# Optimization experiments

Measured on AMD Instinct MI355X. Metric: run time of the kernel, lower is better.

Reference implementation:

```python
import jax, jax.numpy as jnp
import numpy as np

N_EXPERTS = 8
TOPK = 2


def setup_inputs() -> dict:
    key = jax.random.key(0)
    k1, k2, k3, k4 = jax.random.split(key, 4)
    B, T, D, H, E = 2, 2048, 1024, 4096, N_EXPERTS
    s = 1.0 / np.sqrt(D)
    return {
        "x": jax.random.normal(k1, (B, T, D), dtype=jnp.float32),
        "W_gate": jax.random.normal(k2, (E, D), dtype=jnp.float32) * s,
        "W_fc": jax.random.normal(k3, (E, H, D), dtype=jnp.float32) * s,
        "W_proj": jax.random.normal(k4, (E, D, H), dtype=jnp.float32) * (1.0 / np.sqrt(H)),
    }


def reference(x, W_gate, W_fc, W_proj):
    B, T, D = x.shape
    E = W_gate.shape[0]
    N = B * T
    xf = x.reshape(N, D)

    # gating
    gate_logits = xf @ W_gate.T                       # [N, E]
    gate_probs = jax.nn.softmax(gate_logits, axis=-1)
    rw, eidx = jax.lax.top_k(gate_probs, TOPK)        # [N, K]
    rw = rw / jnp.sum(rw, axis=-1, keepdims=True)

    # exact dispatch: out[n] = sum_k rw[n,k] * MLP_{eidx[n,k]}(x[n])
    # loop over the small fixed expert count; each expert processes all tokens,
    # masked-combined by its per-token routing weight (same math as index_add dispatch).
    out = jnp.zeros_like(xf)
    for e in range(E):
        we = jnp.sum(jnp.where(eidx == e, rw, 0.0), axis=-1)     # [N]
        h = jnp.square(jax.nn.relu(xf @ W_fc[e].T))              # relu(x)^2, [N, H]
        out = out + (h @ W_proj[e].T) * we[:, None]

    # load-balance loss
    ones = jnp.ones((N * TOPK,), dtype=gate_probs.dtype)
    counts = jax.ops.segment_sum(ones, eidx.reshape(-1), num_segments=E)
    expert_freq = counts / N
    balance_loss = jnp.sum(gate_probs.mean(axis=0) * jax.lax.stop_gradient(expert_freq)) * E

    return out.reshape(B, T, D), balance_loss
```

## Files before the change

### kernel.cpp

```cpp
#include <hip/hip_runtime.h>
#include <hip/hip_bf16.h>
#include <math.h>

#define N_TOK 4096
#define D_DIM 1024
#define H_DIM 4096
#define E_NUM 8
#define NSLOT (N_TOK * 2)

typedef short bf16x8 __attribute__((ext_vector_type(8)));
typedef float f32x4 __attribute__((ext_vector_type(4)));


__device__ __forceinline__ unsigned short f2bf(float f) {
  unsigned int u = __float_as_uint(f);
  u += 0x7FFFu + ((u >> 16) & 1u);
  return (unsigned short)(u >> 16);
}

__device__ __forceinline__ void gld_lds16(const void* g, void* l) {
  __builtin_amdgcn_global_load_lds(
      (__attribute__((address_space(1))) void*)(g),
      (__attribute__((address_space(3))) void*)(l), 16, 0, 0);
}


__global__ void zero_init(float* __restrict__ p, int n4, int* __restrict__ ctrl) {
  int i = blockIdx.x * blockDim.x + threadIdx.x;
  if (i < n4) ((float4*)p)[i] = make_float4(0.f, 0.f, 0.f, 0.f);
  if (blockIdx.x == 0 && threadIdx.x < 64) ctrl[threadIdx.x] = 0;
}

__global__ void cvt_weights(const float* __restrict__ wfc, const float* __restrict__ wproj,
                            unsigned short* __restrict__ wfcb, unsigned short* __restrict__ wpjb) {
  const int L = 8388608;
  const int stride = gridDim.x * blockDim.x;
  for (int i = blockIdx.x * blockDim.x + threadIdx.x; i < 2 * L; i += stride) {
    const bool first = (i < L);
    const int j = first ? i : i - L;
    float4 v = first ? ((const float4*)wfc)[j] : ((const float4*)wproj)[j];
    ushort4 o;
    o.x = f2bf(v.x); o.y = f2bf(v.y); o.z = f2bf(v.z); o.w = f2bf(v.w);
    if (first) ((ushort4*)wfcb)[j] = o; else ((ushort4*)wpjb)[j] = o;
  }
}


__global__ void gating_kernel(const float* __restrict__ x,
                              const float* __restrict__ wg,
                              float* __restrict__ probs,
                              int* __restrict__ eidx,
                              float* __restrict__ rw,
                              unsigned short* __restrict__ xb) {
  __shared__ float4 wg_lds[2048];
  const int t = threadIdx.x;
  const int lane = t & 63;
  const int wave = t >> 6;

#pragma unroll
  for (int j = 0; j < 8; ++j)
    wg_lds[t + 256 * j] = ((const float4*)wg)[t + 256 * j];
  __syncthreads();

#pragma unroll
  for (int j = 0; j < 4; ++j) {
    const int n = blockIdx.x * 16 + wave * 4 + j;
    const float4* xr = (const float4*)(x + (size_t)n * D_DIM);
    ushort4* xw = (ushort4*)(xb + (size_t)n * D_DIM);

    float acc[E_NUM];
#pragma unroll
    for (int e = 0; e < E_NUM; ++e) acc[e] = 0.f;

#pragma unroll
    for (int i = 0; i < 4; ++i) {
      float4 xv = xr[lane + 64 * i];
      ushort4 xo;
      xo.x = f2bf(xv.x); xo.y = f2bf(xv.y); xo.z = f2bf(xv.z); xo.w = f2bf(xv.w);
      xw[lane + 64 * i] = xo;
#pragma unroll
      for (int e = 0; e < E_NUM; ++e) {
        float4 wv = wg_lds[e * 256 + lane + 64 * i];
        acc[e] += xv.x * wv.x + xv.y * wv.y + xv.z * wv.z + xv.w * wv.w;
      }
    }
#pragma unroll
    for (int m = 1; m < 64; m <<= 1) {
#pragma unroll
      for (int e = 0; e < E_NUM; ++e) acc[e] += __shfl_xor(acc[e], m, 64);
    }

    float mx = acc[0];
#pragma unroll
    for (int e = 1; e < E_NUM; ++e) mx = fmaxf(mx, acc[e]);
    float p[E_NUM], s = 0.f;
#pragma unroll
    for (int e = 0; e < E_NUM; ++e) { p[e] = __expf(acc[e] - mx); s += p[e]; }
    float inv = 1.f / s;

    if (lane < E_NUM) probs[(size_t)n * E_NUM + lane] = p[lane] * inv;

    if (lane == 0) {
      int i1 = 0;
#pragma unroll
      for (int e = 1; e < E_NUM; ++e) if (p[e] > p[i1]) i1 = e;
      int i2 = (i1 == 0) ? 1 : 0;
#pragma unroll
      for (int e = 0; e < E_NUM; ++e)
        if (e != i1 && p[e] > p[i2]) i2 = e;
      float p1 = p[i1], p2 = p[i2];
      float wsum = 1.f / (p1 + p2);
      eidx[n] = i1 | (i2 << 8);
      rw[2 * n] = p1 * wsum;
      rw[2 * n + 1] = p2 * wsum;
    }
  }
}

__global__ void reduce_route(const float* __restrict__ probs,
                             const int* __restrict__ eidx,
                             int* __restrict__ counts,
                             int* __restrict__ offsets,
                             float* __restrict__ loss) {
  const int t = threadIdx.x;
  float4 part = make_float4(0.f, 0.f, 0.f, 0.f);
  for (int j = 0; j < 32; ++j) {
    float4 v = ((const float4*)probs)[t + 256 * j];
    part.x += v.x; part.y += v.y; part.z += v.z; part.w += v.w;
  }
  int cnt[E_NUM];
#pragma unroll
  for (int e = 0; e < E_NUM; ++e) cnt[e] = 0;
  for (int j = 0; j < 16; ++j) {
    int pk = eidx[t + 256 * j];
    int e1 = pk & 255, e2 = pk >> 8;
#pragma unroll
    for (int e = 0; e < E_NUM; ++e) cnt[e] += (e1 == e) + (e2 == e);
  }

  __shared__ float redf[256 * E_NUM];
  __shared__ int redi[256 * E_NUM];
  const int eb = (t & 1) * 4;
#pragma unroll
  for (int e = 0; e < E_NUM; ++e) { redf[t * E_NUM + e] = 0.f; redi[t * E_NUM + e] = cnt[e]; }
  redf[t * E_NUM + eb + 0] = part.x;
  redf[t * E_NUM + eb + 1] = part.y;
  redf[t * E_NUM + eb + 2] = part.z;
  redf[t * E_NUM + eb + 3] = part.w;
  __syncthreads();
  for (int s = 128; s > 0; s >>= 1) {
    if (t < s) {
#pragma unroll
      for (int e = 0; e < E_NUM; ++e) {
        redf[t * E_NUM + e] += redf[(t + s) * E_NUM + e];
        redi[t * E_NUM + e] += redi[(t + s) * E_NUM + e];
      }
    }
    __syncthreads();
  }
  if (t == 0) {
    int o = 0;
    float L = 0.f;
    for (int e = 0; e < E_NUM; ++e) {
      int c = redi[e];
      counts[e] = c;
      offsets[e] = o;
      o += c;
      L += redf[e] * (float)c;
    }
    loss[0] = L * (float)E_NUM / ((float)N_TOK * (float)N_TOK);
  }
}

__global__ void scatter_kernel(const int* __restrict__ eidx, const float* __restrict__ rw,
                               const int* __restrict__ offsets, int* __restrict__ cursor,
                               int* __restrict__ tok_id, float* __restrict__ tok_w) {
  __shared__ int lcnt[E_NUM];
  __shared__ int lbase[E_NUM];
  const int t = threadIdx.x;
  const int n = blockIdx.x * 256 + t;
  if (t < E_NUM) lcnt[t] = 0;
  __syncthreads();
  int pk = eidx[n];
  int e1 = pk & 255, e2 = pk >> 8;
  int p1 = atomicAdd(&lcnt[e1], 1);
  int p2 = atomicAdd(&lcnt[e2], 1);
  __syncthreads();
  if (t < E_NUM) lbase[t] = atomicAdd(&cursor[t], lcnt[t]);
  __syncthreads();
  int d1 = offsets[e1] + lbase[e1] + p1;
  tok_id[d1] = n; tok_w[d1] = rw[2 * n];
  int d2 = offsets[e2] + lbase[e2] + p2;
  tok_id[d2] = n; tok_w[d2] = rw[2 * n + 1];
}


__launch_bounds__(256, 2)
__global__ void gemm_fc(const unsigned short* __restrict__ xb,
                        const unsigned short* __restrict__ wfc,
                        const int* __restrict__ tok_id,
                        const int* __restrict__ counts,
                        const int* __restrict__ offsets,
                        unsigned short* __restrict__ hbuf) {
  const int e = blockIdx.z;
  const int cnt = counts[e];
  const int mtile = blockIdx.y;
  if (mtile * 128 >= cnt) return;
  const int ntile = blockIdx.x;
  const int off = offsets[e];

  __shared__ __align__(16) unsigned short As[128 * 64];
  __shared__ __align__(16) unsigned short Bs[128 * 64];

  const int t = threadIdx.x;
  const int lane = t & 63;
  const int wave = t >> 6;
  const int wm = (wave >> 1) * 64;
  const int wn = (wave & 1) * 64;
  const int srow = t >> 3;
  const int seg = (t & 7) ^ (srow & 7);

  const unsigned short* aptr[4];
  const unsigned short* bptr[4];
#pragma unroll
  for (int p = 0; p < 4; ++p) {
    int r = mtile * 128 + p * 32 + srow;
    r = (r < cnt) ? r : (cnt - 1);
    int tok = tok_id[off + r];
    aptr[p] = xb + (size_t)tok * D_DIM + seg * 8;
    int br = ntile * 128 + p * 32 + srow;
    bptr[p] = wfc + ((size_t)e * H_DIM + br) * D_DIM + seg * 8;
  }

  f32x4 acc[4][4];
#pragma unroll
  for (int i = 0; i < 4; ++i)
#pragma unroll
    for (int j = 0; j < 4; ++j) acc[i][j] = (f32x4){0.f, 0.f, 0.f, 0.f};

  const int frow_a = wm + (lane & 15);
  const int frow_b = wn + (lane & 15);
  const int q = lane >> 4;
  const int csw = lane & 7;

  for (int k0 = 0; k0 < D_DIM; k0 += 64) {
#pragma unroll
    for (int p = 0; p < 4; ++p) {
      gld_lds16(aptr[p] + k0, &As[p * 2048 + t * 8]);
      gld_lds16(bptr[p] + k0, &Bs[p * 2048 + t * 8]);
    }
    __syncthreads();
#pragma unroll
    for (int kk = 0; kk < 64; kk += 32) {
      const int ca = ((((kk >> 3) + q) ^ csw) << 3);
      bf16x8 af[4], bfr[4];
#pragma unroll
      for (int i = 0; i < 4; ++i)
        af[i] = *(const bf16x8*)&As[(frow_a + i * 16) * 64 + ca];
#pragma unroll
      for (int j = 0; j < 4; ++j)
        bfr[j] = *(const bf16x8*)&Bs[(frow_b + j * 16) * 64 + ca];
#pragma unroll
      for (int i = 0; i < 4; ++i)
#pragma unroll
        for (int j = 0; j < 4; ++j)
          acc[i][j] = __builtin_amdgcn_mfma_f32_16x16x32_bf16(af[i], bfr[j], acc[i][j], 0, 0, 0);
    }
    __syncthreads();
  }

  const int lm = (lane >> 4) * 4;
  const int ln = lane & 15;
#pragma unroll
  for (int i = 0; i < 4; ++i) {
#pragma unroll
    for (int r = 0; r < 4; ++r) {
      int m = mtile * 128 + wm + i * 16 + lm + r;
      if (m < cnt) {
        size_t rowbase = (size_t)(off + m) * H_DIM + ntile * 128 + wn;
#pragma unroll
        for (int j = 0; j < 4; ++j) {
          float v = acc[i][j][r];
          v = v > 0.f ? v * v : 0.f;
          hbuf[rowbase + j * 16 + ln] = f2bf(v);
        }
      }
    }
  }
}

__launch_bounds__(256, 2)
__global__ void gemm_proj(const unsigned short* __restrict__ hbuf,
                          const unsigned short* __restrict__ wproj,
                          const int* __restrict__ tok_id,
                          const float* __restrict__ tok_w,
                          const int* __restrict__ counts,
                          const int* __restrict__ offsets,
                          float* __restrict__ out) {
  const int e = blockIdx.z >> 2;
  const int kbase = (blockIdx.z & 3) * (H_DIM / 4);
  const int cnt = counts[e];
  const int mtile = blockIdx.y;
  if (mtile * 128 >= cnt) return;
  const int ntile = blockIdx.x;
  const int off = offsets[e];

  __shared__ __align__(16) unsigned short As[128 * 64];
  __shared__ __align__(16) unsigned short Bs[128 * 64];

  const int t = threadIdx.x;
  const int lane = t & 63;
  const int wave = t >> 6;
  const int wm = (wave >> 1) * 64;
  const int wn = (wave & 1) * 64;
  const int srow = t >> 3;
  const int seg = (t & 7) ^ (srow & 7);

  const unsigned short* aptr[4];
  const unsigned short* bptr[4];
#pragma unroll
  for (int p = 0; p < 4; ++p) {
    int r = mtile * 128 + p * 32 + srow;
    r = (r < cnt) ? r : (cnt - 1);
    aptr[p] = hbuf + (size_t)(off + r) * H_DIM + seg * 8;
    int br = ntile * 128 + p * 32 + srow;
    bptr[p] = wproj + ((size_t)e * D_DIM + br) * H_DIM + seg * 8;
  }

  f32x4 acc[4][4];
#pragma unroll
  for (int i = 0; i < 4; ++i)
#pragma unroll
    for (int j = 0; j < 4; ++j) acc[i][j] = (f32x4){0.f, 0.f, 0.f, 0.f};

  const int frow_a = wm + (lane & 15);
  const int frow_b = wn + (lane & 15);
  const int q = lane >> 4;
  const int csw = lane & 7;

  for (int k0 = kbase; k0 < kbase + H_DIM / 4; k0 += 64) {
#pragma unroll
    for (int p = 0; p < 4; ++p) {
      gld_lds16(aptr[p] + k0, &As[p * 2048 + t * 8]);
      gld_lds16(bptr[p] + k0, &Bs[p * 2048 + t * 8]);
    }
    __syncthreads();
#pragma unroll
    for (int kk = 0; kk < 64; kk += 32) {
      const int ca = ((((kk >> 3) + q) ^ csw) << 3);
      bf16x8 af[4], bfr[4];
#pragma unroll
      for (int i = 0; i < 4; ++i)
        af[i] = *(const bf16x8*)&As[(frow_a + i * 16) * 64 + ca];
#pragma unroll
      for (int j = 0; j < 4; ++j)
        bfr[j] = *(const bf16x8*)&Bs[(frow_b + j * 16) * 64 + ca];
#pragma unroll
      for (int i = 0; i < 4; ++i)
#pragma unroll
        for (int j = 0; j < 4; ++j)
          acc[i][j] = __builtin_amdgcn_mfma_f32_16x16x32_bf16(af[i], bfr[j], acc[i][j], 0, 0, 0);
    }
    __syncthreads();
  }

  const int lm = (lane >> 4) * 4;
  const int ln = lane & 15;
#pragma unroll
  for (int i = 0; i < 4; ++i) {
#pragma unroll
    for (int r = 0; r < 4; ++r) {
      int m = mtile * 128 + wm + i * 16 + lm + r;
      if (m < cnt) {
        int slot = off + m;
        float w = tok_w[slot];
        float* orow = out + (size_t)tok_id[slot] * D_DIM + ntile * 128 + wn;
#pragma unroll
        for (int j = 0; j < 4; ++j)
          atomicAdd(&orow[j * 16 + ln], acc[i][j][r] * w);
      }
    }
  }
}


extern "C" void kernel_launch(void* const* d_in, const int* in_sizes, int n_in,
                              void* d_out, int out_size, void* d_ws, size_t ws_size,
                              hipStream_t stream) {
  (void)in_sizes; (void)n_in; (void)out_size; (void)ws_size;
  const float* x = (const float*)d_in[0];
  const float* wg = (const float*)d_in[1];
  const float* wfc = (const float*)d_in[2];
  const float* wproj = (const float*)d_in[3];
  float* out = (float*)d_out;
  char* ws = (char*)d_ws;

  int* counts = (int*)(ws + 0);
  int* cursor = (int*)(ws + 64);
  int* offsets = (int*)(ws + 128);
  int* eidx = (int*)(ws + 256);
  float* rw = (float*)(ws + 16640);
  int* tok_id = (int*)(ws + 49408);
  float* tok_w = (float*)(ws + 82176);
  float* probs = (float*)(ws + 114944);
  unsigned short* xb = (unsigned short*)(ws + 246016);
  unsigned short* wfcb = (unsigned short*)(ws + 8634624);
  unsigned short* wpjb = (unsigned short*)(ws + 75743488);
  unsigned short* hbuf = (unsigned short*)(ws + 142852352);

  hipLaunchKernelGGL(zero_init, dim3(4096), dim3(256), 0, stream, out, 1048576, (int*)ws);
  hipLaunchKernelGGL(cvt_weights, dim3(32768), dim3(256), 0, stream, wfc, wproj, wfcb, wpjb);
  hipLaunchKernelGGL(gating_kernel, dim3(256), dim3(256), 0, stream, x, wg, probs, eidx, rw, xb);
  hipLaunchKernelGGL(reduce_route, dim3(1), dim3(256), 0, stream, probs, eidx, counts, offsets, out + 4194304);
  hipLaunchKernelGGL(scatter_kernel, dim3(16), dim3(256), 0, stream, eidx, rw, offsets, cursor, tok_id, tok_w);
  hipLaunchKernelGGL(gemm_fc, dim3(32, 32, 8), dim3(256), 0, stream, xb, wfcb, tok_id, counts, offsets, hbuf);
  hipLaunchKernelGGL(gemm_proj, dim3(8, 32, 32), dim3(256), 0, stream, hbuf, wpjb, tok_id, tok_w, counts, offsets, out);
}
```

Baseline: 586.4 us.

## Fold routing reduction into gating, widen weight conversion, halve proj split-K

The single-block reduce_route kernel is removed. Per-expert counts and probability sums are now accumulated with shared then global atomics inside the gating kernel, and offsets and the balance loss are computed in the scatter and GEMM kernels. Weight conversion now handles 8 elements per thread with a 4x smaller grid, and the projection GEMM splits K two ways instead of four. The aim is to cut one serial launch, the probs round trip, and half of the output atomics, at the cost of fewer blocks in the projection GEMM and nondeterministic float atomic ordering.

```diff
diff --git a/kernel.cpp b/kernel.cpp
--- a/kernel.cpp
+++ b/kernel.cpp
@@ -24,6 +24,12 @@
       (__attribute__((address_space(3))) void*)(l), 16, 0, 0);
 }
 
+__device__ __forceinline__ int expert_off(const int* __restrict__ counts, int e) {
+  int o = 0;
+  for (int i = 0; i < e; ++i) o += counts[i];
+  return o;
+}
+
 
 __global__ void zero_init(float* __restrict__ p, int n4, int* __restrict__ ctrl) {
   int i = blockIdx.x * blockDim.x + threadIdx.x;
@@ -33,30 +39,38 @@
 
 __global__ void cvt_weights(const float* __restrict__ wfc, const float* __restrict__ wproj,
                             unsigned short* __restrict__ wfcb, unsigned short* __restrict__ wpjb) {
-  const int L = 8388608;
+  const int U = 4194304;
   const int stride = gridDim.x * blockDim.x;
-  for (int i = blockIdx.x * blockDim.x + threadIdx.x; i < 2 * L; i += stride) {
-    const bool first = (i < L);
-    const int j = first ? i : i - L;
-    float4 v = first ? ((const float4*)wfc)[j] : ((const float4*)wproj)[j];
-    ushort4 o;
-    o.x = f2bf(v.x); o.y = f2bf(v.y); o.z = f2bf(v.z); o.w = f2bf(v.w);
-    if (first) ((ushort4*)wfcb)[j] = o; else ((ushort4*)wpjb)[j] = o;
+  for (int i = blockIdx.x * blockDim.x + threadIdx.x; i < 2 * U; i += stride) {
+    const bool first = (i < U);
+    const int j = first ? i : i - U;
+    const float4* s = ((const float4*)(first ? wfc : wproj)) + 2 * (size_t)j;
+    float4 a = s[0], b = s[1];
+    bf16x8 o;
+    o[0] = (short)f2bf(a.x); o[1] = (short)f2bf(a.y);
+    o[2] = (short)f2bf(a.z); o[3] = (short)f2bf(a.w);
+    o[4] = (short)f2bf(b.x); o[5] = (short)f2bf(b.y);
+    o[6] = (short)f2bf(b.z); o[7] = (short)f2bf(b.w);
+    ((bf16x8*)(first ? wfcb : wpjb))[j] = o;
   }
 }
 
 
 __global__ void gating_kernel(const float* __restrict__ x,
                               const float* __restrict__ wg,
-                              float* __restrict__ probs,
                               int* __restrict__ eidx,
                               float* __restrict__ rw,
-                              unsigned short* __restrict__ xb) {
+                              unsigned short* __restrict__ xb,
+                              int* __restrict__ counts,
+                              float* __restrict__ sumP) {
   __shared__ float4 wg_lds[2048];
+  __shared__ int lhist[E_NUM];
+  __shared__ float lsum[E_NUM];
   const int t = threadIdx.x;
   const int lane = t & 63;
   const int wave = t >> 6;
 
+  if (t < E_NUM) { lhist[t] = 0; lsum[t] = 0.f; }
 #pragma unroll
   for (int j = 0; j < 8; ++j)
     wg_lds[t + 256 * j] = ((const float4*)wg)[t + 256 * j];
@@ -98,7 +112,7 @@
     for (int e = 0; e < E_NUM; ++e) { p[e] = __expf(acc[e] - mx); s += p[e]; }
     float inv = 1.f / s;
 
-    if (lane < E_NUM) probs[(size_t)n * E_NUM + lane] = p[lane] * inv;
+    if (lane < E_NUM) atomicAdd(&lsum[lane], p[lane] * inv);
 
     if (lane == 0) {
       int i1 = 0;
@@ -113,73 +127,38 @@
       eidx[n] = i1 | (i2 << 8);
       rw[2 * n] = p1 * wsum;
       rw[2 * n + 1] = p2 * wsum;
-    }
-  }
-}
-
-__global__ void reduce_route(const float* __restrict__ probs,
-                             const int* __restrict__ eidx,
-                             int* __restrict__ counts,
-                             int* __restrict__ offsets,
-                             float* __restrict__ loss) {
-  const int t = threadIdx.x;
-  float4 part = make_float4(0.f, 0.f, 0.f, 0.f);
-  for (int j = 0; j < 32; ++j) {
-    float4 v = ((const float4*)probs)[t + 256 * j];
-    part.x += v.x; part.y += v.y; part.z += v.z; part.w += v.w;
-  }
-  int cnt[E_NUM];
-#pragma unroll
-  for (int e = 0; e < E_NUM; ++e) cnt[e] = 0;
-  for (int j = 0; j < 16; ++j) {
-    int pk = eidx[t + 256 * j];
-    int e1 = pk & 255, e2 = pk >> 8;
-#pragma unroll
-    for (int e = 0; e < E_NUM; ++e) cnt[e] += (e1 == e) + (e2 == e);
-  }
-
-  __shared__ float redf[256 * E_NUM];
-  __shared__ int redi[256 * E_NUM];
-  const int eb = (t & 1) * 4;
-#pragma unroll
-  for (int e = 0; e < E_NUM; ++e) { redf[t * E_NUM + e] = 0.f; redi[t * E_NUM + e] = cnt[e]; }
-  redf[t * E_NUM + eb + 0] = part.x;
-  redf[t * E_NUM + eb + 1] = part.y;
-  redf[t * E_NUM + eb + 2] = part.z;
-  redf[t * E_NUM + eb + 3] = part.w;
-  __syncthreads();
-  for (int s = 128; s > 0; s >>= 1) {
-    if (t < s) {
-#pragma unroll
-      for (int e = 0; e < E_NUM; ++e) {
-        redf[t * E_NUM + e] += redf[(t + s) * E_NUM + e];
-        redi[t * E_NUM + e] += redi[(t + s) * E_NUM + e];
-      }
-    }
-    __syncthreads();
-  }
-  if (t == 0) {
-    int o = 0;
-    float L = 0.f;
-    for (int e = 0; e < E_NUM; ++e) {
-      int c = redi[e];
-      counts[e] = c;
-      offsets[e] = o;
-      o += c;
-      L += redf[e] * (float)c;
-    }
-    loss[0] = L * (float)E_NUM / ((float)N_TOK * (float)N_TOK);
+      atomicAdd(&lhist[i1], 1);
+      atomicAdd(&lhist[i2], 1);
+    }
+  }
+  __syncthreads();
+  if (t < E_NUM) {
+    atomicAdd(&counts[t], lhist[t]);
+    atomicAdd(&sumP[t], lsum[t]);
   }
 }
 
 __global__ void scatter_kernel(const int* __restrict__ eidx, const float* __restrict__ rw,
-                               const int* __restrict__ offsets, int* __restrict__ cursor,
-                               int* __restrict__ tok_id, float* __restrict__ tok_w) {
+                               const int* __restrict__ counts, const float* __restrict__ sumP,
+                               int* __restrict__ cursor,
+                               int* __restrict__ tok_id, float* __restrict__ tok_w,
+                               float* __restrict__ loss) {
   __shared__ int lcnt[E_NUM];
   __shared__ int lbase[E_NUM];
+  __shared__ int soff[E_NUM];
   const int t = threadIdx.x;
   const int n = blockIdx.x * 256 + t;
-  if (t < E_NUM) lcnt[t] = 0;
+  if (t < E_NUM) {
+    lcnt[t] = 0;
+    int o = 0;
+    for (int i = 0; i < t; ++i) o += counts[i];
+    soff[t] = o;
+  }
+  if (blockIdx.x == 0 && t == 0) {
+    float L = 0.f;
+    for (int e = 0; e < E_NUM; ++e) L += sumP[e] * (float)counts[e];
+    loss[0] = L * (float)E_NUM / ((float)N_TOK * (float)N_TOK);
+  }
   __syncthreads();
   int pk = eidx[n];
   int e1 = pk & 255, e2 = pk >> 8;
@@ -188,9 +167,9 @@
   __syncthreads();
   if (t < E_NUM) lbase[t] = atomicAdd(&cursor[t], lcnt[t]);
   __syncthreads();
-  int d1 = offsets[e1] + lbase[e1] + p1;
+  int d1 = soff[e1] + lbase[e1] + p1;
   tok_id[d1] = n; tok_w[d1] = rw[2 * n];
-  int d2 = offsets[e2] + lbase[e2] + p2;
+  int d2 = soff[e2] + lbase[e2] + p2;
   tok_id[d2] = n; tok_w[d2] = rw[2 * n + 1];
 }
 
@@ -200,14 +179,13 @@
                         const unsigned short* __restrict__ wfc,
                         const int* __restrict__ tok_id,
                         const int* __restrict__ counts,
-                        const int* __restrict__ offsets,
                         unsigned short* __restrict__ hbuf) {
   const int e = blockIdx.z;
   const int cnt = counts[e];
   const int mtile = blockIdx.y;
   if (mtile * 128 >= cnt) return;
   const int ntile = blockIdx.x;
-  const int off = offsets[e];
+  const int off = expert_off(counts, e);
 
   __shared__ __align__(16) unsigned short As[128 * 64];
   __shared__ __align__(16) unsigned short Bs[128 * 64];
@@ -295,15 +273,14 @@
                           const int* __restrict__ tok_id,
                           const float* __restrict__ tok_w,
                           const int* __restrict__ counts,
-                          const int* __restrict__ offsets,
                           float* __restrict__ out) {
-  const int e = blockIdx.z >> 2;
-  const int kbase = (blockIdx.z & 3) * (H_DIM / 4);
+  const int e = blockIdx.z >> 1;
+  const int kbase = (blockIdx.z & 1) * (H_DIM / 2);
   const int cnt = counts[e];
   const int mtile = blockIdx.y;
   if (mtile * 128 >= cnt) return;
   const int ntile = blockIdx.x;
-  const int off = offsets[e];
+  const int off = expert_off(counts, e);
 
   __shared__ __align__(16) unsigned short As[128 * 64];
   __shared__ __align__(16) unsigned short Bs[128 * 64];
@@ -338,7 +315,7 @@
   const int q = lane >> 4;
   const int csw = lane & 7;
 
-  for (int k0 = kbase; k0 < kbase + H_DIM / 4; k0 += 64) {
+  for (int k0 = kbase; k0 < kbase + H_DIM / 2; k0 += 64) {
 #pragma unroll
     for (int p = 0; p < 4; ++p) {
       gld_lds16(aptr[p] + k0, &As[p * 2048 + t * 8]);
@@ -397,22 +374,20 @@
 
   int* counts = (int*)(ws + 0);
   int* cursor = (int*)(ws + 64);
-  int* offsets = (int*)(ws + 128);
+  float* sumP = (float*)(ws + 192);
   int* eidx = (int*)(ws + 256);
   float* rw = (float*)(ws + 16640);
   int* tok_id = (int*)(ws + 49408);
   float* tok_w = (float*)(ws + 82176);
-  float* probs = (float*)(ws + 114944);
   unsigned short* xb = (unsigned short*)(ws + 246016);
   unsigned short* wfcb = (unsigned short*)(ws + 8634624);
   unsigned short* wpjb = (unsigned short*)(ws + 75743488);
   unsigned short* hbuf = (unsigned short*)(ws + 142852352);
 
   hipLaunchKernelGGL(zero_init, dim3(4096), dim3(256), 0, stream, out, 1048576, (int*)ws);
-  hipLaunchKernelGGL(cvt_weights, dim3(32768), dim3(256), 0, stream, wfc, wproj, wfcb, wpjb);
-  hipLaunchKernelGGL(gating_kernel, dim3(256), dim3(256), 0, stream, x, wg, probs, eidx, rw, xb);
-  hipLaunchKernelGGL(reduce_route, dim3(1), dim3(256), 0, stream, probs, eidx, counts, offsets, out + 4194304);
-  hipLaunchKernelGGL(scatter_kernel, dim3(16), dim3(256), 0, stream, eidx, rw, offsets, cursor, tok_id, tok_w);
-  hipLaunchKernelGGL(gemm_fc, dim3(32, 32, 8), dim3(256), 0, stream, xb, wfcb, tok_id, counts, offsets, hbuf);
-  hipLaunchKernelGGL(gemm_proj, dim3(8, 32, 32), dim3(256), 0, stream, hbuf, wpjb, tok_id, tok_w, counts, offsets, out);
-}
+  hipLaunchKernelGGL(cvt_weights, dim3(4096), dim3(256), 0, stream, wfc, wproj, wfcb, wpjb);
+  hipLaunchKernelGGL(gating_kernel, dim3(256), dim3(256), 0, stream, x, wg, eidx, rw, xb, counts, sumP);
+  hipLaunchKernelGGL(scatter_kernel, dim3(16), dim3(256), 0, stream, eidx, rw, counts, sumP, cursor, tok_id, tok_w, out + 4194304);
+  hipLaunchKernelGGL(gemm_fc, dim3(32, 32, 8), dim3(256), 0, stream, xb, wfcb, tok_id, counts, hbuf);
+  hipLaunchKernelGGL(gemm_proj, dim3(8, 32, 16), dim3(256), 0, stream, hbuf, wpjb, tok_id, tok_w, counts, out);
+}
```

Result: faster. 563.4 us (-3.9%).
